# Kernel tuning notes

Measured on AMD Instinct MI355X. Metric: run time of the kernel, lower is better.

The kernel has to match this reference:

```python
import jax, jax.numpy as jnp
import numpy as np


def setup_inputs() -> dict:
    key = jax.random.key(0)
    x = jax.random.normal(key, (32, 1024, 1024), dtype=jnp.float32)
    return {"x": x}


def reference(x) -> jnp.ndarray:
    # Orthonormal DCT-II along axis 1 via length-2n FFT of [x, reverse(x)],
    # matching tf dct_odd_case numerics (complex64 path, real part taken).
    N, n, m = x.shape
    nf = jnp.float32(n)
    # y = [x; flip(x, axis=1)] -> length 2n along axis 1
    y = jnp.concatenate([x, x[:, ::-1, :]], axis=1)
    F = jnp.fft.fft(y.astype(jnp.complex64), axis=1)[:, :n, :]  # [N, n, m] complex64
    k = jnp.arange(n, dtype=jnp.float32)
    # twiddle: exp(-i*pi*k/(2n)) / sqrt(2n), with k=0 term divided by sqrt(2)
    phase = -k * (jnp.pi / (2.0 * nf))
    t = (jnp.cos(phase) + 1j * jnp.sin(phase)).astype(jnp.complex64) / jnp.sqrt(2.0 * nf)
    scale0 = jnp.where(k == 0, 1.0 / jnp.sqrt(jnp.float32(2.0)), jnp.float32(1.0))
    t = t * scale0.astype(jnp.complex64)
    dct_x = jnp.real(t[None, :, None] * F)  # [N, n, m] float32
    return dct_x
```

## Files before the change

### kernel.cpp

```cpp
#include <hip/hip_runtime.h>
#include <hip/hip_bf16.h>
#include <math.h>

typedef __bf16 bf16_8 __attribute__((ext_vector_type(8)));
typedef __bf16 bf16_4 __attribute__((ext_vector_type(4)));
typedef float f32x4 __attribute__((ext_vector_type(4)));

#define NDIM 1024

__device__ static inline void async_copy16(const void* g, void* l) {
  __builtin_amdgcn_global_load_lds(
      (__attribute__((address_space(1))) void*)g,
      (__attribute__((address_space(3))) void*)l, 16, 0, 0);
}


__global__ void gen_dct_fold(__bf16* __restrict__ A) {
  int idx = blockIdx.x * blockDim.x + threadIdx.x;
  int sel = idx >> 15;
  int rem = idx & 32767;
  int mp = rem >> 6;
  int slot = rem & 63;
  int kt = slot >> 3, s = slot & 7;
  int k = 2 * mp + sel;
  int r = mp & 127, mtp = mp >> 7;
  float sc = (k == 0) ? 0.03125f : 0.04419417382415922f;
  int jb = kt * 64 + s * 8;
  bf16_8 v;
#pragma unroll
  for (int q = 0; q < 8; q++) {
    int j = jb + q;
    int t = (k * (2 * j + 1)) & 4095;
    float ang = (float)t * 1.5339807878856412e-3f;
    v[q] = (__bf16)(sc * cosf(ang));
  }
  *(bf16_8*)(A + (((size_t)(sel * 32 + mtp * 8 + kt)) << 13) + r * 64 +
             ((s ^ (r & 7)) << 3)) = v;
}

__global__ __launch_bounds__(256) void fold_cvt(const float* __restrict__ x,
                                                __bf16* __restrict__ B) {
  __shared__ __bf16 Tu[64 * 128];
  __shared__ __bf16 Tv[64 * 128];
  const int t = threadIdx.x;
  const int kt = blockIdx.x, nt = blockIdx.y, b = blockIdx.z;
  const float* xb = x + (size_t)b * (NDIM * NDIM) + nt * 128;
  const int kr = t >> 5;
  const int c4 = (t & 31) * 4;
  const int jb = kt * 64;
  const int mb = 1023 - kt * 64;
#pragma unroll
  for (int u = 0; u < 8; u++) {
    int k = u * 8 + kr;
    f32x4 a = *(const f32x4*)(xb + (size_t)(jb + k) * NDIM + c4);
    f32x4 m = *(const f32x4*)(xb + (size_t)(mb - k) * NDIM + c4);
    f32x4 su = a + m, dv = a - m;
    bf16_4 wu, wv;
#pragma unroll
    for (int i = 0; i < 4; i++) {
      wu[i] = (__bf16)su[i];
      wv[i] = (__bf16)dv[i];
    }
    *(bf16_4*)(&Tu[k * 128 + c4]) = wu;
    *(bf16_4*)(&Tv[k * 128 + c4]) = wv;
  }
  __syncthreads();
  __bf16* outU = B + (((size_t)(b * 2 + 0) * 64 + nt * 8 + kt) << 13);
  __bf16* outV = B + (((size_t)(b * 2 + 1) * 64 + nt * 8 + kt) << 13);
#pragma unroll
  for (int u = 0; u < 4; u++) {
    int c = t * 4 + u;
    int r = c >> 3, sp = c & 7;
    int s = sp ^ (r & 7);
    bf16_8 vU, vV;
#pragma unroll
    for (int q = 0; q < 8; q++) {
      vU[q] = Tu[(s * 8 + q) * 128 + r];
      vV[q] = Tv[(s * 8 + q) * 128 + r];
    }
    *(bf16_8*)(outU + c * 8) = vU;
    *(bf16_8*)(outV + c * 8) = vV;
  }
}

__global__ __launch_bounds__(256) void dct_gemm3(const __bf16* __restrict__ A,
                                                 const __bf16* __restrict__ B,
                                                 float* __restrict__ out) {
  __shared__ __align__(1024) __bf16 As[2][128 * 64];
  __shared__ __align__(1024) __bf16 Bs[2][128 * 64];
  const int t = threadIdx.x;
  const int w = t >> 6, lane = t & 63;
  const int nt = blockIdx.x, b = blockIdx.z;
  const int sel = blockIdx.y & 1, mtp = blockIdx.y >> 1;

  const __bf16* ag =
      A + (((size_t)(sel * 32 + mtp * 8)) << 13) + w * 2048 + lane * 8;
  const __bf16* bg =
      B + (((size_t)(b * 2 + sel) * 64 + nt * 8) << 13) + w * 2048 + lane * 8;

  const int r16 = lane & 15;
  const int g8 = (lane >> 4) << 3;
  const int wm = (w & 1) << 6, wn = (w >> 1) << 6;
  const int xr = (r16 & 7) << 3;
  const int kof0 = g8 ^ xr;
  const int kof1 = (32 + g8) ^ xr;

#pragma unroll
  for (int i = 0; i < 4; i++) {
    async_copy16(ag + i * 512, &As[0][w * 2048 + i * 512]);
    async_copy16(bg + i * 512, &Bs[0][w * 2048 + i * 512]);
  }
  __syncthreads();

  f32x4 acc[4][4] = {};

  for (int kt = 0; kt < 8; kt++) {
    const int cur = kt & 1;
    if (kt < 7) {
      const __bf16* an = ag + (size_t)(kt + 1) * 8192;
      const __bf16* bn = bg + (size_t)(kt + 1) * 8192;
      const int nb = cur ^ 1;
#pragma unroll
      for (int i = 0; i < 4; i++) {
        async_copy16(an + i * 512, &As[nb][w * 2048 + i * 512]);
        async_copy16(bn + i * 512, &Bs[nb][w * 2048 + i * 512]);
      }
    }
    const __bf16* as = &As[cur][0];
    const __bf16* bs = &Bs[cur][0];
#pragma unroll
    for (int h = 0; h < 2; h++) {
      const int kof = h ? kof1 : kof0;
      bf16_8 af[4], bfr[4];
#pragma unroll
      for (int i = 0; i < 4; i++)
        af[i] = *(const bf16_8*)(as + (wm + i * 16 + r16) * 64 + kof);
#pragma unroll
      for (int j = 0; j < 4; j++)
        bfr[j] = *(const bf16_8*)(bs + (wn + j * 16 + r16) * 64 + kof);
#pragma unroll
      for (int i = 0; i < 4; i++)
#pragma unroll
        for (int j = 0; j < 4; j++)
          acc[i][j] = __builtin_amdgcn_mfma_f32_16x16x32_bf16(af[i], bfr[j],
                                                              acc[i][j], 0, 0, 0);
    }
    __syncthreads();
  }

  float* ob = out + (size_t)b * (NDIM * NDIM);
  const int rbase = (lane >> 4) << 2;
  const int cofs = lane & 15;
  const int n0 = nt * 128;
#pragma unroll
  for (int i = 0; i < 4; i++)
#pragma unroll
    for (int rr = 0; rr < 4; rr++) {
      int rh = mtp * 128 + wm + i * 16 + rbase + rr;
      int row = rh * 2 + sel;
#pragma unroll
      for (int j = 0; j < 4; j++) {
        int col = n0 + wn + j * 16 + cofs;
        ob[(size_t)row * NDIM + col] = acc[i][j][rr];
      }
    }
}

#define BM 128
#define BN 128
#define BK 32
#define BSTRIDE 40

__global__ void gen_dct_mat(__bf16* __restrict__ C) {
  int idx = blockIdx.x * blockDim.x + threadIdx.x;
  int k = idx >> 10;
  int j = idx & 1023;
  int t = (k * (2 * j + 1)) & 4095;
  float ang = (float)t * 1.5339807878856412e-3f;
  float s = (k == 0) ? 0.03125f : 0.04419417382415922f;
  C[idx] = (__bf16)(s * cosf(ang));
}

__global__ __launch_bounds__(256) void dct_gemm(
    const float* __restrict__ x, const __bf16* __restrict__ A,
    float* __restrict__ out) {
  __shared__ __align__(64) __bf16 Asm[BM * BK];
  __shared__ __align__(64) __bf16 Bsm[BN * BSTRIDE];

  const int t = threadIdx.x;
  const int wave = t >> 6;
  const int lane = t & 63;
  const int bb = blockIdx.z;
  const int m0 = blockIdx.y * BM;
  const int n0 = blockIdx.x * BN;

  const __bf16* Ag0 =
      A + (size_t)(m0 + wave * 16 + (lane >> 2)) * NDIM + ((lane & 3) * 8);
  const __bf16* Ag1 = Ag0 + (size_t)64 * NDIM;
  __bf16* Al0 = Asm + (wave * 16) * BK;
  __bf16* Al1 = Asm + (64 + wave * 16) * BK;

  const int bc = t & 127;
  const int bjg = t >> 7;
  const float* xs =
      x + (size_t)bb * (NDIM * NDIM) + (size_t)(bjg * 16) * NDIM + (n0 + bc);
  bf16_8* bs0 = (bf16_8*)(Bsm + bc * BSTRIDE + bjg * 16);
  bf16_8* bs1 = (bf16_8*)(Bsm + bc * BSTRIDE + bjg * 16 + 8);

  const int row16 = lane & 15;
  const int kq8 = (lane >> 4) * 8;
  const int wm = (wave & 1) * 64;
  const int wn = (wave >> 1) * 64;

  f32x4 acc[4][4] = {};

  for (int k0 = 0; k0 < NDIM; k0 += BK) {
    __syncthreads();
    async_copy16(Ag0 + k0, Al0);
    async_copy16(Ag1 + k0, Al1);

    const float* xp = xs + (size_t)k0 * NDIM;
    bf16_8 v0, v1;
#pragma unroll
    for (int q = 0; q < 8; q++) {
      v0[q] = (__bf16)xp[(size_t)q * NDIM];
      v1[q] = (__bf16)xp[(size_t)(q + 8) * NDIM];
    }
    *bs0 = v0;
    *bs1 = v1;
    __syncthreads();

    bf16_8 af[4], bfr[4];
#pragma unroll
    for (int i = 0; i < 4; i++)
      af[i] = *(const bf16_8*)(Asm + (wm + i * 16 + row16) * BK + kq8);
#pragma unroll
    for (int j = 0; j < 4; j++)
      bfr[j] = *(const bf16_8*)(Bsm + (wn + j * 16 + row16) * BSTRIDE + kq8);
#pragma unroll
    for (int i = 0; i < 4; i++)
#pragma unroll
      for (int j = 0; j < 4; j++)
        acc[i][j] = __builtin_amdgcn_mfma_f32_16x16x32_bf16(af[i], bfr[j],
                                                            acc[i][j], 0, 0, 0);
  }

  float* ob = out + (size_t)bb * (NDIM * NDIM);
  const int rbase = (lane >> 4) * 4;
  const int cofs = lane & 15;
#pragma unroll
  for (int i = 0; i < 4; i++) {
#pragma unroll
    for (int r = 0; r < 4; r++) {
      int row = m0 + wm + i * 16 + rbase + r;
#pragma unroll
      for (int j = 0; j < 4; j++) {
        int col = n0 + wn + j * 16 + cofs;
        ob[(size_t)row * NDIM + col] = acc[i][j][r];
      }
    }
  }
}

extern "C" void kernel_launch(void* const* d_in, const int* in_sizes, int n_in,
                              void* d_out, int out_size, void* d_ws,
                              size_t ws_size, hipStream_t stream) {
  const float* x = (const float*)d_in[0];
  float* out = (float*)d_out;

  const size_t need = (size_t)66 * 1024 * 1024;
  if (ws_size >= need) {
    __bf16* Ab = (__bf16*)d_ws;
    __bf16* Bb = (__bf16*)((char*)d_ws + (size_t)2 * 1024 * 1024);
    gen_dct_fold<<<dim3(256), dim3(256), 0, stream>>>(Ab);
    fold_cvt<<<dim3(8, 8, 32), dim3(256), 0, stream>>>(x, Bb);
    dct_gemm3<<<dim3(8, 8, 32), dim3(256), 0, stream>>>(Ab, Bb, out);
  } else {
    __bf16* Cmat = (__bf16*)d_ws;
    gen_dct_mat<<<dim3((NDIM * NDIM) / 256), dim3(256), 0, stream>>>(Cmat);
    dct_gemm<<<dim3(NDIM / BN, NDIM / BM, 32), dim3(256), 0, stream>>>(x, Cmat,
                                                                       out);
  }
}
```

Measured before the change: 279.7 us.

## Read DCT matrix fragments directly from global memory and pad fold transpose buffer

The GEMM kernel no longer stages the small shared DCT coefficient matrix A through LDS. Each wave now loads its A fragments straight from global memory, which is expected to hit in cache since all blocks reuse it. This halves LDS use and adds a launch_bounds occupancy hint of 4 blocks. The fold/convert kernel's LDS transpose buffers get a row stride of 132 instead of 128 to cut bank conflicts on the strided column reads. The risk is that the global A loads now sit directly in the MFMA loop without async prefetch, so their latency may be exposed.

```diff
diff --git a/kernel.cpp b/kernel.cpp
--- a/kernel.cpp
+++ b/kernel.cpp
@@ -38,10 +38,11 @@
              ((s ^ (r & 7)) << 3)) = v;
 }
 
+#define TFP 132
 __global__ __launch_bounds__(256) void fold_cvt(const float* __restrict__ x,
                                                 __bf16* __restrict__ B) {
-  __shared__ __bf16 Tu[64 * 128];
-  __shared__ __bf16 Tv[64 * 128];
+  __shared__ __bf16 Tu[64 * TFP];
+  __shared__ __bf16 Tv[64 * TFP];
   const int t = threadIdx.x;
   const int kt = blockIdx.x, nt = blockIdx.y, b = blockIdx.z;
   const float* xb = x + (size_t)b * (NDIM * NDIM) + nt * 128;
@@ -61,8 +62,8 @@
       wu[i] = (__bf16)su[i];
       wv[i] = (__bf16)dv[i];
     }
-    *(bf16_4*)(&Tu[k * 128 + c4]) = wu;
-    *(bf16_4*)(&Tv[k * 128 + c4]) = wv;
+    *(bf16_4*)(&Tu[k * TFP + c4]) = wu;
+    *(bf16_4*)(&Tv[k * TFP + c4]) = wv;
   }
   __syncthreads();
   __bf16* outU = B + (((size_t)(b * 2 + 0) * 64 + nt * 8 + kt) << 13);
@@ -75,26 +76,23 @@
     bf16_8 vU, vV;
 #pragma unroll
     for (int q = 0; q < 8; q++) {
-      vU[q] = Tu[(s * 8 + q) * 128 + r];
-      vV[q] = Tv[(s * 8 + q) * 128 + r];
+      vU[q] = Tu[(s * 8 + q) * TFP + r];
+      vV[q] = Tv[(s * 8 + q) * TFP + r];
     }
     *(bf16_8*)(outU + c * 8) = vU;
     *(bf16_8*)(outV + c * 8) = vV;
   }
 }
 
-__global__ __launch_bounds__(256) void dct_gemm3(const __bf16* __restrict__ A,
-                                                 const __bf16* __restrict__ B,
-                                                 float* __restrict__ out) {
-  __shared__ __align__(1024) __bf16 As[2][128 * 64];
+__global__ __launch_bounds__(256, 4) void dct_gemm4(
+    const __bf16* __restrict__ A, const __bf16* __restrict__ B,
+    float* __restrict__ out) {
   __shared__ __align__(1024) __bf16 Bs[2][128 * 64];
   const int t = threadIdx.x;
   const int w = t >> 6, lane = t & 63;
   const int nt = blockIdx.x, b = blockIdx.z;
   const int sel = blockIdx.y & 1, mtp = blockIdx.y >> 1;
 
-  const __bf16* ag =
-      A + (((size_t)(sel * 32 + mtp * 8)) << 13) + w * 2048 + lane * 8;
   const __bf16* bg =
       B + (((size_t)(b * 2 + sel) * 64 + nt * 8) << 13) + w * 2048 + lane * 8;
 
@@ -105,11 +103,12 @@
   const int kof0 = g8 ^ xr;
   const int kof1 = (32 + g8) ^ xr;
 
-#pragma unroll
-  for (int i = 0; i < 4; i++) {
-    async_copy16(ag + i * 512, &As[0][w * 2048 + i * 512]);
+  const __bf16* agf =
+      A + (((size_t)(sel * 32 + mtp * 8)) << 13) + (size_t)(wm + r16) * 64;
+
+#pragma unroll
+  for (int i = 0; i < 4; i++)
     async_copy16(bg + i * 512, &Bs[0][w * 2048 + i * 512]);
-  }
   __syncthreads();
 
   f32x4 acc[4][4] = {};
@@ -117,16 +116,12 @@
   for (int kt = 0; kt < 8; kt++) {
     const int cur = kt & 1;
     if (kt < 7) {
-      const __bf16* an = ag + (size_t)(kt + 1) * 8192;
       const __bf16* bn = bg + (size_t)(kt + 1) * 8192;
-      const int nb = cur ^ 1;
-#pragma unroll
-      for (int i = 0; i < 4; i++) {
-        async_copy16(an + i * 512, &As[nb][w * 2048 + i * 512]);
-        async_copy16(bn + i * 512, &Bs[nb][w * 2048 + i * 512]);
-      }
-    }
-    const __bf16* as = &As[cur][0];
+#pragma unroll
+      for (int i = 0; i < 4; i++)
+        async_copy16(bn + i * 512, &Bs[cur ^ 1][w * 2048 + i * 512]);
+    }
+    const __bf16* as = agf + (size_t)kt * 8192;
     const __bf16* bs = &Bs[cur][0];
 #pragma unroll
     for (int h = 0; h < 2; h++) {
@@ -134,7 +129,7 @@
       bf16_8 af[4], bfr[4];
 #pragma unroll
       for (int i = 0; i < 4; i++)
-        af[i] = *(const bf16_8*)(as + (wm + i * 16 + r16) * 64 + kof);
+        af[i] = *(const bf16_8*)(as + i * 1024 + kof);
 #pragma unroll
       for (int j = 0; j < 4; j++)
         bfr[j] = *(const bf16_8*)(bs + (wn + j * 16 + r16) * 64 + kof);
@@ -274,7 +269,7 @@
     __bf16* Bb = (__bf16*)((char*)d_ws + (size_t)2 * 1024 * 1024);
     gen_dct_fold<<<dim3(256), dim3(256), 0, stream>>>(Ab);
     fold_cvt<<<dim3(8, 8, 32), dim3(256), 0, stream>>>(x, Bb);
-    dct_gemm3<<<dim3(8, 8, 32), dim3(256), 0, stream>>>(Ab, Bb, out);
+    dct_gemm4<<<dim3(8, 8, 32), dim3(256), 0, stream>>>(Ab, Bb, out);
   } else {
     __bf16* Cmat = (__bf16*)d_ws;
     gen_dct_mat<<<dim3((NDIM * NDIM) / 256), dim3(256), 0, stream>>>(Cmat);
```

Measured after the change: 298.1 us. 1.07x slower.
